# Kernel tuning notes

Measured on AMD Instinct MI355X. Metric: run time of the kernel, lower is better.

Reference implementation:

```python
import jax, jax.numpy as jnp
import numpy as np

B, S, W = 128, 256, 1
DEPTH = 655            # MathTypeKeysMax
UNITS = 128
PROBLEM_BUCKETS = 32


def setup_inputs() -> dict:
    key = jax.random.key(0)
    ks = jax.random.split(key, 14)
    ri = lambda k, shape, hi: jax.random.randint(k, shape, 0, hi, dtype=jnp.int32)
    K = 4 * DEPTH * W  # flattened per-timestep feature width = 2620
    return {
        'move_count': ri(ks[0], (B,), 100),
        'moves_remaining': ri(ks[1], (B,), 100),
        'last_rule': ri(ks[2], (B,), 12),
        'node_count': ri(ks[3], (B,), 64),
        'problem_type': ri(ks[4], (B,), PROBLEM_BUCKETS),
        'bwd_vectors': ri(ks[5], (B, S, W), DEPTH),
        'fwd_vectors': ri(ks[6], (B, S, W), DEPTH),
        'last_bwd_vectors': ri(ks[7], (B, S, W), DEPTH),
        'last_fwd_vectors': ri(ks[8], (B, S, W), DEPTH),
        'W_dense': jax.random.normal(ks[9], (K, UNITS), jnp.float32) * (1.0 / np.sqrt(K)),
        'b_dense': jnp.zeros((UNITS,), jnp.float32),
        'Wx': jax.random.normal(ks[10], (UNITS, 4 * UNITS), jnp.float32) * (1.0 / np.sqrt(UNITS)),
        'Wh': jax.random.normal(ks[11], (UNITS, 4 * UNITS), jnp.float32) * (1.0 / np.sqrt(UNITS)),
        'b_lstm': jnp.zeros((4 * UNITS,), jnp.float32),
    }


def _lstm(x, Wx, Wh, b):
    # x: [B, S, U] -> (seq hidden [B, S, U], final hidden [B, U]); keras gate order i,f,c,o
    U = Wh.shape[0]
    bsz = x.shape[0]
    # precompute input projections once: [S, B, 4U]
    xz = jnp.einsum('bsu,uv->sbv', x, Wx) + b

    def step(carry, zt):
        h, c = carry
        z = zt + h @ Wh
        i, f, g, o = jnp.split(z, 4, axis=-1)
        i = jax.nn.sigmoid(i)
        f = jax.nn.sigmoid(f)
        g = jnp.tanh(g)
        o = jax.nn.sigmoid(o)
        c = f * c + i * g
        h = o * jnp.tanh(c)
        return (h, c), h

    init = (jnp.zeros((bsz, U), x.dtype), jnp.zeros((bsz, U), x.dtype))
    (h_last, _), hs = jax.lax.scan(step, init, xz)
    return jnp.transpose(hs, (1, 0, 2)), h_last


def reference(move_count, moves_remaining, last_rule, node_count, problem_type,
              bwd_vectors, fwd_vectors, last_bwd_vectors, last_fwd_vectors,
              W_dense, b_dense, Wx, Wh, b_lstm):
    f32 = lambda a: a.astype(jnp.float32)
    # DenseFeatures context extraction: 3 numeric int columns + 32-bucket indicator
    context_inputs = jnp.concatenate([
        f32(last_rule)[:, None],
        f32(move_count)[:, None],
        f32(node_count)[:, None],
        jax.nn.one_hot(problem_type, PROBLEM_BUCKETS, dtype=jnp.float32),
    ], axis=-1)  # [B, 35]

    sequence_length = bwd_vectors.shape[1]
    # one-hot each [B,S,W] sequence to [B,S,W,DEPTH], concat on last axis -> [B,S,W,4*DEPTH]
    oh = jnp.concatenate([
        jax.nn.one_hot(bwd_vectors, DEPTH, dtype=jnp.float32),
        jax.nn.one_hot(fwd_vectors, DEPTH, dtype=jnp.float32),
        jax.nn.one_hot(last_bwd_vectors, DEPTH, dtype=jnp.float32),
        jax.nn.one_hot(last_fwd_vectors, DEPTH, dtype=jnp.float32),
    ], axis=-1)
    bsz = oh.shape[0]
    # per-example Flatten keeps leading S dim, so the loop == one batched matmul
    flat = oh.reshape(bsz, sequence_length, -1)      # [B, S, 4*DEPTH*W]
    outputs = jnp.einsum('bsk,ku->bsu', flat, W_dense) + b_dense  # [B, S, U]

    hidden_states, lstm_vectors = _lstm(outputs, Wx, Wh, b_lstm)
    return (context_inputs, lstm_vectors, hidden_states, sequence_length)
```

## Files before the change

### kernel.cpp

```cpp
#include <hip/hip_runtime.h>
#include <cstdint>

#define BB   128
#define SS   256
#define NDEPTH 655
#define UU   128
#define VV   512
#define NPB  32

__global__ void context_kernel(const int* __restrict__ last_rule,
                               const int* __restrict__ move_count,
                               const int* __restrict__ node_count,
                               const int* __restrict__ problem_type,
                               float* __restrict__ out, int write_seq) {
    int i = blockIdx.x * blockDim.x + threadIdx.x;
    if (i < BB * 35) {
        int b = i / 35, c = i % 35;
        float v;
        if (c == 0)      v = (float)last_rule[b];
        else if (c == 1) v = (float)move_count[b];
        else if (c == 2) v = (float)node_count[b];
        else             v = (problem_type[b] == (c - 3)) ? 1.0f : 0.0f;
        out[i] = v;
    }
    if (write_seq && i == 0)
        out[(size_t)BB*35 + (size_t)BB*UU + (size_t)BB*SS*UU] = (float)SS;
}

__global__ void wdwx_kernel(const float* __restrict__ Wd,
                            const float* __restrict__ Wx,
                            const float* __restrict__ b_dense,
                            const float* __restrict__ b_lstm,
                            float* __restrict__ WdWx,
                            float* __restrict__ base) {
    int v  = threadIdx.x;
    int k0 = blockIdx.x * 4;
    const float* wd0 = Wd + (size_t)k0 * UU;
    float a0 = 0.f, a1 = 0.f, a2 = 0.f, a3 = 0.f;
    for (int u = 0; u < UU; ++u) {
        float wx = Wx[u * VV + v];
        a0 = fmaf(wd0[u],        wx, a0);
        a1 = fmaf(wd0[UU + u],   wx, a1);
        a2 = fmaf(wd0[2*UU + u], wx, a2);
        a3 = fmaf(wd0[3*UU + u], wx, a3);
    }
    WdWx[(size_t)(k0+0)*VV + v] = a0;
    WdWx[(size_t)(k0+1)*VV + v] = a1;
    WdWx[(size_t)(k0+2)*VV + v] = a2;
    WdWx[(size_t)(k0+3)*VV + v] = a3;
    if (blockIdx.x == 0) {
        float a = 0.f;
        for (int u = 0; u < UU; ++u) a = fmaf(b_dense[u], Wx[u * VV + v], a);
        base[v] = a + b_lstm[v];
    }
}

__global__ __launch_bounds__(512, 2)
void lstm_kernel(const int* __restrict__ bwd,  const int* __restrict__ fwd,
                 const int* __restrict__ lbwd, const int* __restrict__ lfwd,
                 const float* __restrict__ WdWx,
                 const float* __restrict__ base,
                 const float* __restrict__ Wh,
                 float* __restrict__ hidden_states,
                 float* __restrict__ lstm_vectors) {
    const int b    = blockIdx.x;
    const int t    = threadIdx.x;
    const int lane = t & 63;
    const int w    = t >> 6;
    const int gate = lane & 3;
    const int u    = w * 16 + (lane >> 2);
    const int col  = gate * UU + u;

    __shared__ __align__(16) float h_buf[2][UU];
    __shared__ int idx_lds[SS][4];

    float wh[UU];
    #pragma unroll
    for (int k = 0; k < UU; ++k) wh[k] = Wh[k * VV + col];

    for (int s = t; s < SS; s += 512) {
        idx_lds[s][0] =            bwd [b*SS + s];
        idx_lds[s][1] =   NDEPTH + fwd [b*SS + s];
        idx_lds[s][2] = 2*NDEPTH + lbwd[b*SS + s];
        idx_lds[s][3] = 3*NDEPTH + lfwd[b*SS + s];
    }
    if (t < UU) h_buf[0][t] = 0.0f;
    float c    = 0.0f;
    float bias = base[col];
    __syncthreads();

    float g0 = WdWx[(size_t)idx_lds[0][0] * VV + col];
    float g1 = WdWx[(size_t)idx_lds[0][1] * VV + col];
    float g2 = WdWx[(size_t)idx_lds[0][2] * VV + col];
    float g3 = WdWx[(size_t)idx_lds[0][3] * VV + col];

    int p = 0;
    for (int s = 0; s < SS; ++s) {
        float z = bias + (g0 + g1) + (g2 + g3);
        if (s + 1 < SS) {
            g0 = WdWx[(size_t)idx_lds[s+1][0] * VV + col];
            g1 = WdWx[(size_t)idx_lds[s+1][1] * VV + col];
            g2 = WdWx[(size_t)idx_lds[s+1][2] * VV + col];
            g3 = WdWx[(size_t)idx_lds[s+1][3] * VV + col];
        }

        const float* hb = h_buf[p];
        float z0 = 0.f, z1 = 0.f, z2 = 0.f, z3 = 0.f;
        #pragma unroll
        for (int k = 0; k < UU; k += 4) {
            float4 hv = *(const float4*)(hb + k);
            z0 = fmaf(hv.x, wh[k],   z0);
            z1 = fmaf(hv.y, wh[k+1], z1);
            z2 = fmaf(hv.z, wh[k+2], z2);
            z3 = fmaf(hv.w, wh[k+3], z3);
        }
        z += (z0 + z1) + (z2 + z3);

        float xs = (gate == 2) ? 2.0f * z : z;
        float sg = __fdividef(1.0f, 1.0f + __expf(-xs));
        float a  = (gate == 2) ? 2.0f * sg - 1.0f : sg;

        float v1 = __shfl_xor(a, 1);
        float v2 = __shfl_xor(a, 2);
        float v3 = __shfl_xor(v1, 2);
        float ig = (gate & 1) ? v1 * v3 : a * v2;
        float gf = (gate & 1) ? ((gate & 2) ? v2 : a)
                              : ((gate & 2) ? v3 : v1);
        float go = (gate & 1) ? ((gate & 2) ? a  : v2)
                              : ((gate & 2) ? v1 : v3);
        c = fmaf(gf, c, ig);
        float e  = __expf(2.0f * c);
        float tc = 1.0f - __fdividef(2.0f, e + 1.0f);
        float h  = go * tc;

        if (gate == 0) {
            h_buf[p ^ 1][u] = h;
            hidden_states[((size_t)b * SS + s) * UU + u] = h;
        }
        __syncthreads();
        p ^= 1;
    }
    if (t < UU) lstm_vectors[(size_t)b * UU + t] = h_buf[p][t];
}

extern "C" void kernel_launch(void* const* d_in, const int* in_sizes, int n_in,
                              void* d_out, int out_size, void* d_ws, size_t ws_size,
                              hipStream_t stream) {
    const int* move_count   = (const int*)d_in[0];
    const int* last_rule    = (const int*)d_in[2];
    const int* node_count   = (const int*)d_in[3];
    const int* problem_type = (const int*)d_in[4];
    const int* bwd          = (const int*)d_in[5];
    const int* fwd          = (const int*)d_in[6];
    const int* lbwd         = (const int*)d_in[7];
    const int* lfwd         = (const int*)d_in[8];
    const float* Wd         = (const float*)d_in[9];
    const float* b_dense    = (const float*)d_in[10];
    const float* Wx         = (const float*)d_in[11];
    const float* Wh         = (const float*)d_in[12];
    const float* b_lstm     = (const float*)d_in[13];

    float* out  = (float*)d_out;
    float* WdWx = (float*)d_ws;
    float* base = WdWx + (size_t)(4 * NDEPTH) * VV;

    float* lstm_out = out + BB * 35;
    float* hs_out   = lstm_out + BB * UU;
    int write_seq = (out_size > BB*35 + BB*UU + BB*SS*UU) ? 1 : 0;

    context_kernel<<<(BB*35 + 255)/256, 256, 0, stream>>>(
        last_rule, move_count, node_count, problem_type, out, write_seq);
    wdwx_kernel<<<NDEPTH, VV, 0, stream>>>(Wd, Wx, b_dense, b_lstm, WdWx, base);
    lstm_kernel<<<BB, 512, 0, stream>>>(bwd, fwd, lbwd, lfwd, WdWx, base, Wh,
                                        hs_out, lstm_out);
}
```

Measured before the change: 366.2 us.

## Split recurrent matvec across quad lanes by k-slice with shuffle reduction

Each of the four lanes in a quad now handles one 32-wide slice of the hidden vector for all four gates of its unit, rather than the full 128-wide dot product for a single gate. Partial sums are combined with two rounds of xor-shuffles. The h buffer is padded to 36-float strides so the four lanes read different LDS regions, and each lane reads a quarter as much LDS per step. The cost is extra shuffles and adds on the serial recurrence path.

```diff
diff --git a/kernel.cpp b/kernel.cpp
--- a/kernel.cpp
+++ b/kernel.cpp
@@ -67,16 +67,20 @@
     const int t    = threadIdx.x;
     const int lane = t & 63;
     const int w    = t >> 6;
-    const int gate = lane & 3;
+    const int q    = lane & 3;
     const int u    = w * 16 + (lane >> 2);
-    const int col  = gate * UU + u;
-
-    __shared__ __align__(16) float h_buf[2][UU];
+    const int col  = q * UU + u;
+
+    __shared__ __align__(16) float h_buf[2][144];
     __shared__ int idx_lds[SS][4];
 
-    float wh[UU];
+    float wh[128];
     #pragma unroll
-    for (int k = 0; k < UU; ++k) wh[k] = Wh[k * VV + col];
+    for (int kk = 0; kk < 32; ++kk) {
+        #pragma unroll
+        for (int g = 0; g < 4; ++g)
+            wh[kk*4+g] = Wh[(size_t)(32*q + kk) * VV + g*UU + u];
+    }
 
     for (int s = t; s < SS; s += 512) {
         idx_lds[s][0] =            bwd [b*SS + s];
@@ -84,7 +88,7 @@
         idx_lds[s][2] = 2*NDEPTH + lbwd[b*SS + s];
         idx_lds[s][3] = 3*NDEPTH + lfwd[b*SS + s];
     }
-    if (t < UU) h_buf[0][t] = 0.0f;
+    if (t < UU) h_buf[0][36*(t>>5) + (t&31)] = 0.0f;
     float c    = 0.0f;
     float bias = base[col];
     __syncthreads();
@@ -93,6 +97,9 @@
     float g1 = WdWx[(size_t)idx_lds[0][1] * VV + col];
     float g2 = WdWx[(size_t)idx_lds[0][2] * VV + col];
     float g3 = WdWx[(size_t)idx_lds[0][3] * VV + col];
+
+    const bool b0 = (q & 1) != 0;
+    const bool b1 = (q & 2) != 0;
 
     int p = 0;
     for (int s = 0; s < SS; ++s) {
@@ -104,43 +111,63 @@
             g3 = WdWx[(size_t)idx_lds[s+1][3] * VV + col];
         }
 
-        const float* hb = h_buf[p];
-        float z0 = 0.f, z1 = 0.f, z2 = 0.f, z3 = 0.f;
+        const float* hb = h_buf[p] + 36 * q;
+        float pp0 = 0.f, pp1 = 0.f, pp2 = 0.f, pp3 = 0.f;
         #pragma unroll
-        for (int k = 0; k < UU; k += 4) {
-            float4 hv = *(const float4*)(hb + k);
-            z0 = fmaf(hv.x, wh[k],   z0);
-            z1 = fmaf(hv.y, wh[k+1], z1);
-            z2 = fmaf(hv.z, wh[k+2], z2);
-            z3 = fmaf(hv.w, wh[k+3], z3);
+        for (int kk = 0; kk < 32; kk += 4) {
+            float4 hv = *(const float4*)(hb + kk);
+            pp0 = fmaf(hv.x, wh[(kk+0)*4+0], pp0);
+            pp1 = fmaf(hv.x, wh[(kk+0)*4+1], pp1);
+            pp2 = fmaf(hv.x, wh[(kk+0)*4+2], pp2);
+            pp3 = fmaf(hv.x, wh[(kk+0)*4+3], pp3);
+            pp0 = fmaf(hv.y, wh[(kk+1)*4+0], pp0);
+            pp1 = fmaf(hv.y, wh[(kk+1)*4+1], pp1);
+            pp2 = fmaf(hv.y, wh[(kk+1)*4+2], pp2);
+            pp3 = fmaf(hv.y, wh[(kk+1)*4+3], pp3);
+            pp0 = fmaf(hv.z, wh[(kk+2)*4+0], pp0);
+            pp1 = fmaf(hv.z, wh[(kk+2)*4+1], pp1);
+            pp2 = fmaf(hv.z, wh[(kk+2)*4+2], pp2);
+            pp3 = fmaf(hv.z, wh[(kk+2)*4+3], pp3);
+            pp0 = fmaf(hv.w, wh[(kk+3)*4+0], pp0);
+            pp1 = fmaf(hv.w, wh[(kk+3)*4+1], pp1);
+            pp2 = fmaf(hv.w, wh[(kk+3)*4+2], pp2);
+            pp3 = fmaf(hv.w, wh[(kk+3)*4+3], pp3);
         }
-        z += (z0 + z1) + (z2 + z3);
-
-        float xs = (gate == 2) ? 2.0f * z : z;
+
+        float keepA = b0 ? pp1 : pp0;
+        float keepB = b0 ? pp3 : pp2;
+        float sendA = b0 ? pp0 : pp1;
+        float sendB = b0 ? pp2 : pp3;
+        float sA = keepA + __shfl_xor(sendA, 1);
+        float sB = keepB + __shfl_xor(sendB, 1);
+        float send2 = b1 ? sA : sB;
+        z += (b1 ? sB : sA) + __shfl_xor(send2, 2);
+
+        float xs = (q == 2) ? 2.0f * z : z;
         float sg = __fdividef(1.0f, 1.0f + __expf(-xs));
-        float a  = (gate == 2) ? 2.0f * sg - 1.0f : sg;
+        float a  = (q == 2) ? 2.0f * sg - 1.0f : sg;
 
         float v1 = __shfl_xor(a, 1);
         float v2 = __shfl_xor(a, 2);
         float v3 = __shfl_xor(v1, 2);
-        float ig = (gate & 1) ? v1 * v3 : a * v2;
-        float gf = (gate & 1) ? ((gate & 2) ? v2 : a)
-                              : ((gate & 2) ? v3 : v1);
-        float go = (gate & 1) ? ((gate & 2) ? a  : v2)
-                              : ((gate & 2) ? v1 : v3);
+        float ig = (q & 1) ? v1 * v3 : a * v2;
+        float gf = (q & 1) ? ((q & 2) ? v2 : a)
+                           : ((q & 2) ? v3 : v1);
+        float go = (q & 1) ? ((q & 2) ? a  : v2)
+                           : ((q & 2) ? v1 : v3);
         c = fmaf(gf, c, ig);
         float e  = __expf(2.0f * c);
         float tc = 1.0f - __fdividef(2.0f, e + 1.0f);
         float h  = go * tc;
 
-        if (gate == 0) {
-            h_buf[p ^ 1][u] = h;
+        if (q == 0) {
+            h_buf[p ^ 1][36*(u>>5) + (u&31)] = h;
             hidden_states[((size_t)b * SS + s) * UU + u] = h;
         }
         __syncthreads();
         p ^= 1;
     }
-    if (t < UU) lstm_vectors[(size_t)b * UU + t] = h_buf[p][t];
+    if (t < UU) lstm_vectors[(size_t)b * UU + t] = h_buf[p][36*(t>>5) + (t&31)];
 }
 
 extern "C" void kernel_launch(void* const* d_in, const int* in_sizes, int n_in,
```

New measurement: 312.6 us. 14.6% less time.
